# Optimization experiments

Measured on AMD Instinct MI355X. Metric: run time of the kernel, lower is better.

The kernel has to match this reference:

```python
import jax, jax.numpy as jnp
import numpy as np

B, CIN, H, W = 16, 256, 32, 32
COUT = 256
DK = 128       # key depth (total over heads)
DV = 128       # attentional channels (total over heads)
NH = 8
DKH = DK // NH # 16
DVH = DV // NH # 16
CCONV = COUT - DV  # channels of the plain conv branch


def setup_inputs() -> dict:
    key = jax.random.key(0)
    ks = jax.random.split(key, 7)
    x = jax.random.normal(ks[0], (B, CIN, H, W), dtype=jnp.float32)
    # 3x3 conv branch (padding=1), OIHW
    conv_w = jax.random.normal(ks[1], (CCONV, CIN, 3, 3), dtype=jnp.float32) * 0.02
    conv_b = jnp.zeros((CCONV,), dtype=jnp.float32)
    # 1x1 qkv conv, stored as [out, in]
    qkv_w = jax.random.normal(ks[2], (2 * DK + DV, CIN), dtype=jnp.float32) * 0.02
    qkv_b = jnp.zeros((2 * DK + DV,), dtype=jnp.float32)
    # 1x1 output projection for attention branch
    attn_w = jax.random.normal(ks[3], (DV, DV), dtype=jnp.float32) * 0.02
    attn_b = jnp.zeros((DV,), dtype=jnp.float32)
    return {"x": x, "conv_w": conv_w, "conv_b": conv_b,
            "qkv_w": qkv_w, "qkv_b": qkv_b,
            "attn_w": attn_w, "attn_b": attn_b}


def reference(x, conv_w, conv_b, qkv_w, qkv_b, attn_w, attn_b):
    b, _, h, w = x.shape
    hw = h * w
    # plain conv branch: 3x3, padding 1
    conv_out = jax.lax.conv_general_dilated(
        x, conv_w, window_strides=(1, 1), padding=((1, 1), (1, 1)),
        dimension_numbers=("NCHW", "OIHW", "NCHW")) + conv_b[None, :, None, None]
    # 1x1 qkv conv
    qkv = jnp.einsum("bchw,oc->bohw", x, qkv_w) + qkv_b[None, :, None, None]
    q = qkv[:, :DK].reshape(b, NH, DKH, hw) * (DKH ** -0.5)
    k = qkv[:, DK:2 * DK].reshape(b, NH, DKH, hw)
    v = qkv[:, 2 * DK:].reshape(b, NH, DVH, hw)
    # logits[b,n,p,q] = sum_c q[b,n,c,p] * k[b,n,c,q]
    logits = jnp.einsum("bncp,bncq->bnpq", q, k)
    weights = jax.nn.softmax(logits, axis=-1)
    # attn[b,n,c,p] = sum_q v[b,n,c,q] * weights[b,n,p,q]
    attn = jnp.einsum("bncq,bnpq->bncp", v, weights).reshape(b, DV, h, w)
    attn = jnp.einsum("bchw,oc->bohw", attn, attn_w) + attn_b[None, :, None, None]
    return jnp.concatenate((conv_out, attn), axis=1)
```

## Files before the change

kernel.cpp:

```cpp
#include <hip/hip_runtime.h>
#include <cstddef>

#define B_ 16
#define CIN_ 256
#define H_ 32
#define W_ 32
#define HW_ 1024
#define COUT_ 256
#define DK_ 128
#define DV_ 128
#define NH_ 8
#define DKH_ 16
#define DVH_ 16
#define CCONV_ 128
#define QKVO_ 384

typedef __attribute__((ext_vector_type(4))) _Float16 half4v;
typedef __attribute__((ext_vector_type(8))) _Float16 half8v;
typedef __attribute__((ext_vector_type(4))) float float4v;


__global__ __launch_bounds__(256) void xt_kernel(
    const float* __restrict__ x, _Float16* __restrict__ xF)
{
    const int pt = blockIdx.x;
    const int ct = blockIdx.y;
    const int b  = blockIdx.z;
    __shared__ float T[32][33];
    const int t = threadIdx.x;
    const int c = t & 31, r = t >> 5;
#pragma unroll
    for (int i = 0; i < 4; ++i) {
        const int ci = ct * 32 + r + i * 8;
        T[r + i * 8][c] = x[(size_t)(b * CIN_ + ci) * HW_ + pt * 32 + c];
    }
    __syncthreads();
    const int cq = (t & 7) * 4;
    const int pi = t >> 3;
    half4v h;
#pragma unroll
    for (int j = 0; j < 4; ++j) h[j] = (_Float16)T[cq + j][pi];
    const int p = pt * 32 + pi;
    *(half4v*)(xF + ((size_t)(b * 8 + ct) * HW_ + p) * 32 + cq) = h;
}

__global__ __launch_bounds__(256) void wprep_kernel(
    const float* __restrict__ conv_w, const float* __restrict__ qkv_w,
    const float* __restrict__ attn_w, _Float16* __restrict__ wC,
    _Float16* __restrict__ wF, _Float16* __restrict__ wP)
{
    const int bid = blockIdx.x;
    const int t = threadIdx.x;
    if (bid < 128) {
        const int id = bid * 256 + t;
        const int co = id >> 8, ci = id & 255;
        const float* src = conv_w + (size_t)id * 9;
#pragma unroll
        for (int j = 0; j < 9; ++j)
            wC[(((size_t)(ci >> 5) * 9 + j) * 8 + (co >> 4)) * 512 + (co & 15) * 32 + (ci & 31)]
                = (_Float16)src[j];
    } else if (bid < 224) {
        const int g = (bid - 128) * 256 + t;
        const int o = g >> 6, k0 = (g & 63) * 4;
        const float4 v = *(const float4*)(qkv_w + (size_t)o * CIN_ + k0);
        half4v h; h[0] = (_Float16)v.x; h[1] = (_Float16)v.y;
        h[2] = (_Float16)v.z; h[3] = (_Float16)v.w;
        *(half4v*)(wF + ((size_t)(k0 >> 5) * QKVO_ + o) * 32 + (k0 & 31)) = h;
    } else {
        const int g = (bid - 224) * 256 + t;
        const int o = g >> 5, k0 = (g & 31) * 4;
        const float4 v = *(const float4*)(attn_w + (size_t)o * DV_ + k0);
        half4v h; h[0] = (_Float16)v.x; h[1] = (_Float16)v.y;
        h[2] = (_Float16)v.z; h[3] = (_Float16)v.w;
        *(half4v*)(wP + ((size_t)(k0 >> 5) * DV_ + o) * 32 + (k0 & 31)) = h;
    }
}

__global__ __launch_bounds__(256) void qkv_kernel(
    const _Float16* __restrict__ xF, const _Float16* __restrict__ wF,
    const float* __restrict__ qkv_b, _Float16* __restrict__ Qt,
    _Float16* __restrict__ Kt, _Float16* __restrict__ vF)
{
    const int pt = blockIdx.x;
    const int ot = blockIdx.y;
    const int b  = blockIdx.z;
    const int lane = threadIdx.x & 63, w = threadIdx.x >> 6;
    const int l16 = lane & 15, hi = lane >> 4;
    const int p0 = pt * 64;
    const int og = ot * 4 + w;
    const int o0 = og * 16;

    float4v acc[4];
#pragma unroll
    for (int pg = 0; pg < 4; ++pg) acc[pg] = (float4v){0.f, 0.f, 0.f, 0.f};

    for (int kc = 0; kc < 8; ++kc) {
        const half8v a = *(const half8v*)(wF + ((size_t)kc * QKVO_ + o0 + l16) * 32 + hi * 8);
#pragma unroll
        for (int pg = 0; pg < 4; ++pg) {
            const half8v bf = *(const half8v*)(xF + ((size_t)(b * 8 + kc) * HW_ + p0 + pg * 16 + l16) * 32 + hi * 8);
            acc[pg] = __builtin_amdgcn_mfma_f32_16x16x32_f16(a, bf, acc[pg], 0, 0, 0);
        }
    }

    float bias[4];
#pragma unroll
    for (int r = 0; r < 4; ++r) bias[r] = qkv_b[o0 + hi * 4 + r];

    if (og < 16) {
        const float scale = (og < 8) ? 0.25f : 1.0f;
        const int n = og & 7;
        _Float16* dst = (og < 8 ? Qt : Kt) + (size_t)(b * NH_ + n) * (HW_ * 16) + hi * 4;
#pragma unroll
        for (int pg = 0; pg < 4; ++pg) {
            const int p = p0 + pg * 16 + l16;
            half4v h;
#pragma unroll
            for (int r = 0; r < 4; ++r) h[r] = (_Float16)((acc[pg][r] + bias[r]) * scale);
            *(half4v*)(dst + (size_t)p * 16) = h;
        }
    } else {
        const int n = og - 16;
        _Float16* Vb = vF + (size_t)(b * NH_ + n) * (64 * 16 * 16);
#pragma unroll
        for (int pg = 0; pg < 4; ++pg) {
            const int qg = pt * 4 + pg;
#pragma unroll
            for (int r = 0; r < 4; ++r)
                Vb[(size_t)(qg * 16 + hi * 4 + r) * 16 + l16] = (_Float16)(acc[pg][r] + bias[r]);
        }
    }
}

__global__ __launch_bounds__(256) void attn_kernel(
    const _Float16* __restrict__ Qt, const _Float16* __restrict__ Kt,
    const _Float16* __restrict__ vF, _Float16* __restrict__ aF)
{
    const int bx = blockIdx.x;
    const int pc = bx & 3;
    const int n  = (bx >> 2) & 7;
    const int b  = bx >> 5;
    const int lane = threadIdx.x & 63, wave = threadIdx.x >> 6;
    const int l16 = lane & 15, lg = lane >> 4;

    const int bn = b * NH_ + n;
    const _Float16* Qh = Qt + (size_t)bn * (HW_ * 16);
    const _Float16* Kh = Kt + (size_t)bn * (HW_ * 16);
    const _Float16* Vh = vF + (size_t)bn * (64 * 16 * 16);

    const int pbase = pc * 256 + wave * 64;

    half4v qf[4];
#pragma unroll
    for (int t = 0; t < 4; ++t)
        qf[t] = *(const half4v*)(Qh + (size_t)(pbase + t * 16 + l16) * 16 + lg * 4);

    float4v o[4];
    float rs[4];
#pragma unroll
    for (int t = 0; t < 4; ++t) { o[t] = (float4v){0.f, 0.f, 0.f, 0.f}; rs[t] = 0.f; }

    const float4v zero = (float4v){0.f, 0.f, 0.f, 0.f};

    for (int q0 = 0; q0 < HW_; q0 += 16) {
        const half4v kf = *(const half4v*)(Kh + (size_t)(q0 + l16) * 16 + lg * 4);
        const half4v vf = *(const half4v*)(Vh + (size_t)((q0 >> 4) * 16 + l16) * 16 + lg * 4);
#pragma unroll
        for (int t = 0; t < 4; ++t) {
            float4v s = __builtin_amdgcn_mfma_f32_16x16x16f16(kf, qf[t], zero, 0, 0, 0);
            const float e0 = __expf(s[0]);
            const float e1 = __expf(s[1]);
            const float e2 = __expf(s[2]);
            const float e3 = __expf(s[3]);
            rs[t] += (e0 + e1) + (e2 + e3);
            half4v pf;
            pf[0] = (_Float16)e0; pf[1] = (_Float16)e1;
            pf[2] = (_Float16)e2; pf[3] = (_Float16)e3;
            o[t] = __builtin_amdgcn_mfma_f32_16x16x16f16(vf, pf, o[t], 0, 0, 0);
        }
    }
#pragma unroll
    for (int t = 0; t < 4; ++t) {
        float r = rs[t];
        r += __shfl_xor(r, 16);
        r += __shfl_xor(r, 32);
        const float inv = 1.0f / r;
        half4v h;
#pragma unroll
        for (int rr = 0; rr < 4; ++rr) h[rr] = (_Float16)(o[t][rr] * inv);
        *(half4v*)(aF + (((size_t)(b * 64 + (pbase >> 4) + t) * 4 + (n >> 1)) * 16 + l16) * 32
                      + (n & 1) * 16 + lg * 4) = h;
    }
}

__global__ __launch_bounds__(256) void proj_kernel(
    const _Float16* __restrict__ aF, const _Float16* __restrict__ wP,
    const float* __restrict__ attn_b, float* __restrict__ out)
{
    const int pt = blockIdx.x;
    const int ot = blockIdx.y;
    const int b  = blockIdx.z;
    const int lane = threadIdx.x & 63, w = threadIdx.x >> 6;
    const int l16 = lane & 15, hi = lane >> 4;
    const int p0 = pt * 64;
    const int o0 = ot * 64 + w * 16;

    float4v acc[4];
#pragma unroll
    for (int pg = 0; pg < 4; ++pg) acc[pg] = (float4v){0.f, 0.f, 0.f, 0.f};

    for (int kc = 0; kc < 4; ++kc) {
        const half8v a = *(const half8v*)(wP + ((size_t)kc * DV_ + o0 + l16) * 32 + hi * 8);
#pragma unroll
        for (int pg = 0; pg < 4; ++pg) {
            const half8v bf = *(const half8v*)(aF + (((size_t)(b * 64 + pt * 4 + pg) * 4 + kc) * 16 + l16) * 32 + hi * 8);
            acc[pg] = __builtin_amdgcn_mfma_f32_16x16x32_f16(a, bf, acc[pg], 0, 0, 0);
        }
    }
#pragma unroll
    for (int pg = 0; pg < 4; ++pg) {
        const int p = p0 + pg * 16 + l16;
#pragma unroll
        for (int r = 0; r < 4; ++r) {
            const int o = o0 + hi * 4 + r;
            out[((size_t)(b * COUT_ + CCONV_ + o)) * HW_ + p] = acc[pg][r] + attn_b[o];
        }
    }
}

__global__ __launch_bounds__(256) void conv_kernel(
    const _Float16* __restrict__ xF, const _Float16* __restrict__ wC,
    const float* __restrict__ conv_b, float* __restrict__ out)
{
    const int rp = blockIdx.x;
    const int ch = blockIdx.y;
    const int b  = blockIdx.z;
    const int t = threadIdx.x;
    const int lane = t & 63, w = t >> 6;
    const int wc = w & 1, wp = w >> 1;
    const int l16 = lane & 15, hi = lane >> 4;
    const int r = rp * 2 + wp;
    const int coc0 = ch * 4 + wc * 2;

    const bool lane0bad  = (l16 == 0);
    const bool lane15bad = (l16 == 15);
    const half8v z = {0, 0, 0, 0, 0, 0, 0, 0};

    float4v acc[2][2];
#pragma unroll
    for (int i = 0; i < 2; ++i)
#pragma unroll
        for (int j = 0; j < 2; ++j) acc[i][j] = (float4v){0.f, 0.f, 0.f, 0.f};

    for (int kc = 0; kc < 8; ++kc) {
        const _Float16* xk = xF + ((size_t)(b * 8 + kc) * HW_ + r * 32) * 32 + l16 * 32 + hi * 8;
        const _Float16* ab = wC + ((size_t)(kc * 9) * 8 + coc0) * 512 + l16 * 32 + hi * 8;
#pragma unroll
        for (int kh = 0; kh < 3; ++kh) {
            const int rr = r + kh - 1;
            if ((unsigned)rr >= 32u) continue;
#pragma unroll
            for (int kw = 0; kw < 3; ++kw) {
                const _Float16* a = ab + (size_t)((kh * 3 + kw) * 8) * 512;
                const half8v a0 = *(const half8v*)(a);
                const half8v a1 = *(const half8v*)(a + 512);
                const int sh = ((kh - 1) * 32 + (kw - 1)) * 32;
                half8v b0 = *(const half8v*)(xk + sh);
                half8v b1 = *(const half8v*)(xk + sh + 16 * 32);
                if (kw == 0) b0 = lane0bad  ? z : b0;
                if (kw == 2) b1 = lane15bad ? z : b1;
                acc[0][0] = __builtin_amdgcn_mfma_f32_16x16x32_f16(a0, b0, acc[0][0], 0, 0, 0);
                acc[0][1] = __builtin_amdgcn_mfma_f32_16x16x32_f16(a0, b1, acc[0][1], 0, 0, 0);
                acc[1][0] = __builtin_amdgcn_mfma_f32_16x16x32_f16(a1, b0, acc[1][0], 0, 0, 0);
                acc[1][1] = __builtin_amdgcn_mfma_f32_16x16x32_f16(a1, b1, acc[1][1], 0, 0, 0);
            }
        }
    }
#pragma unroll
    for (int cog = 0; cog < 2; ++cog)
#pragma unroll
        for (int rr = 0; rr < 4; ++rr) {
            const int co = (coc0 + cog) * 16 + hi * 4 + rr;
            const float bias = conv_b[co];
            float* dst = out + (size_t)(b * COUT_ + co) * HW_ + r * 32;
            dst[l16]      = acc[cog][0][rr] + bias;
            dst[16 + l16] = acc[cog][1][rr] + bias;
        }
}

extern "C" void kernel_launch(void* const* d_in, const int* in_sizes, int n_in,
                              void* d_out, int out_size, void* d_ws, size_t ws_size,
                              hipStream_t stream)
{
    (void)in_sizes; (void)n_in; (void)out_size; (void)ws_size;
    const float* x      = (const float*)d_in[0];
    const float* conv_w = (const float*)d_in[1];
    const float* conv_b = (const float*)d_in[2];
    const float* qkv_w  = (const float*)d_in[3];
    const float* qkv_b  = (const float*)d_in[4];
    const float* attn_w = (const float*)d_in[5];
    const float* attn_b = (const float*)d_in[6];
    float* out = (float*)d_out;

    char* ws = (char*)d_ws;
    _Float16* xF = (_Float16*)(ws + 4096);
    _Float16* wC = (_Float16*)(ws + 8392704);
    _Float16* wF = (_Float16*)(ws + 8982528);
    _Float16* wP = (_Float16*)(ws + 9179136);
    _Float16* Qt = (_Float16*)(ws + 9211904);
    _Float16* Kt = (_Float16*)(ws + 13406208);
    _Float16* vF = (_Float16*)(ws + 17600512);
    _Float16* aF = (_Float16*)(ws + 21794816);

    xt_kernel<<<dim3(32, 8, B_), dim3(256), 0, stream>>>(x, xF);
    wprep_kernel<<<dim3(240), dim3(256), 0, stream>>>(conv_w, qkv_w, attn_w, wC, wF, wP);
    qkv_kernel<<<dim3(16, 6, B_), dim3(256), 0, stream>>>(xF, wF, qkv_b, Qt, Kt, vF);
    attn_kernel<<<dim3(512), dim3(256), 0, stream>>>(Qt, Kt, vF, aF);
    proj_kernel<<<dim3(16, 2, B_), dim3(256), 0, stream>>>(aF, wP, attn_b, out);
    conv_kernel<<<dim3(16, 2, B_), dim3(256), 0, stream>>>(xF, wC, conv_b, out);
}
```

Measured before the change: 177.3 us.

## Split attention keys across waves, use exp2 softmax, shrink conv tiles for more blocks

The attention kernel now splits the key dimension into two halves handled by paired waves, which doubles the grid to 1024 blocks. The partial outputs and row sums are combined through shared memory before normalization. Q is prescaled by log2(e)/4 so the native exp2 instruction replaces __expf. The conv kernel gives each wave a single 16-channel group on one row and doubles its grid, trading less weight and activation reuse per wave for more parallelism.

New measurement: 186.0 us. 4.9% more time.

```diff
diff --git a/kernel.cpp b/kernel.cpp
--- a/kernel.cpp
+++ b/kernel.cpp
@@ -19,6 +19,7 @@
 typedef __attribute__((ext_vector_type(8))) _Float16 half8v;
 typedef __attribute__((ext_vector_type(4))) float float4v;
 
+#define QSCALE 0.36067376022224085f
 
 __global__ __launch_bounds__(256) void xt_kernel(
     const float* __restrict__ x, _Float16* __restrict__ xF)
@@ -108,7 +109,7 @@
     for (int r = 0; r < 4; ++r) bias[r] = qkv_b[o0 + hi * 4 + r];
 
     if (og < 16) {
-        const float scale = (og < 8) ? 0.25f : 1.0f;
+        const float scale = (og < 8) ? QSCALE : 1.0f;
         const int n = og & 7;
         _Float16* dst = (og < 8 ? Qt : Kt) + (size_t)(b * NH_ + n) * (HW_ * 16) + hi * 4;
 #pragma unroll
@@ -137,10 +138,11 @@
     const _Float16* __restrict__ vF, _Float16* __restrict__ aF)
 {
     const int bx = blockIdx.x;
-    const int pc = bx & 3;
-    const int n  = (bx >> 2) & 7;
-    const int b  = bx >> 5;
+    const int pc = bx & 7;
+    const int n  = (bx >> 3) & 7;
+    const int b  = bx >> 6;
     const int lane = threadIdx.x & 63, wave = threadIdx.x >> 6;
+    const int pg = wave >> 1, qh = wave & 1;
     const int l16 = lane & 15, lg = lane >> 4;
 
     const int bn = b * NH_ + n;
@@ -148,7 +150,7 @@
     const _Float16* Kh = Kt + (size_t)bn * (HW_ * 16);
     const _Float16* Vh = vF + (size_t)bn * (64 * 16 * 16);
 
-    const int pbase = pc * 256 + wave * 64;
+    const int pbase = pc * 128 + pg * 64;
 
     half4v qf[4];
 #pragma unroll
@@ -162,16 +164,17 @@
 
     const float4v zero = (float4v){0.f, 0.f, 0.f, 0.f};
 
-    for (int q0 = 0; q0 < HW_; q0 += 16) {
+    const int q0beg = qh * 512;
+    for (int q0 = q0beg; q0 < q0beg + 512; q0 += 16) {
         const half4v kf = *(const half4v*)(Kh + (size_t)(q0 + l16) * 16 + lg * 4);
         const half4v vf = *(const half4v*)(Vh + (size_t)((q0 >> 4) * 16 + l16) * 16 + lg * 4);
 #pragma unroll
         for (int t = 0; t < 4; ++t) {
             float4v s = __builtin_amdgcn_mfma_f32_16x16x16f16(kf, qf[t], zero, 0, 0, 0);
-            const float e0 = __expf(s[0]);
-            const float e1 = __expf(s[1]);
-            const float e2 = __expf(s[2]);
-            const float e3 = __expf(s[3]);
+            const float e0 = __builtin_amdgcn_exp2f(s[0]);
+            const float e1 = __builtin_amdgcn_exp2f(s[1]);
+            const float e2 = __builtin_amdgcn_exp2f(s[2]);
+            const float e3 = __builtin_amdgcn_exp2f(s[3]);
             rs[t] += (e0 + e1) + (e2 + e3);
             half4v pf;
             pf[0] = (_Float16)e0; pf[1] = (_Float16)e1;
@@ -179,17 +182,37 @@
             o[t] = __builtin_amdgcn_mfma_f32_16x16x16f16(vf, pf, o[t], 0, 0, 0);
         }
     }
-#pragma unroll
-    for (int t = 0; t < 4; ++t) {
-        float r = rs[t];
-        r += __shfl_xor(r, 16);
-        r += __shfl_xor(r, 32);
-        const float inv = 1.0f / r;
-        half4v h;
-#pragma unroll
-        for (int rr = 0; rr < 4; ++rr) h[rr] = (_Float16)(o[t][rr] * inv);
-        *(half4v*)(aF + (((size_t)(b * 64 + (pbase >> 4) + t) * 4 + (n >> 1)) * 16 + l16) * 32
-                      + (n & 1) * 16 + lg * 4) = h;
+
+    __shared__ float Ored[2][64][16];
+    __shared__ float Rred[2][64][4];
+    if (qh == 1) {
+#pragma unroll
+        for (int t = 0; t < 4; ++t) {
+#pragma unroll
+            for (int rr = 0; rr < 4; ++rr) Ored[pg][lane][t * 4 + rr] = o[t][rr];
+            Rred[pg][lane][t] = rs[t];
+        }
+    }
+    __syncthreads();
+    if (qh == 0) {
+#pragma unroll
+        for (int t = 0; t < 4; ++t) {
+#pragma unroll
+            for (int rr = 0; rr < 4; ++rr) o[t][rr] += Ored[pg][lane][t * 4 + rr];
+            rs[t] += Rred[pg][lane][t];
+        }
+#pragma unroll
+        for (int t = 0; t < 4; ++t) {
+            float r = rs[t];
+            r += __shfl_xor(r, 16);
+            r += __shfl_xor(r, 32);
+            const float inv = 1.0f / r;
+            half4v h;
+#pragma unroll
+            for (int rr = 0; rr < 4; ++rr) h[rr] = (_Float16)(o[t][rr] * inv);
+            *(half4v*)(aF + (((size_t)(b * 64 + (pbase >> 4) + t) * 4 + (n >> 1)) * 16 + l16) * 32
+                          + (n & 1) * 16 + lg * 4) = h;
+        }
     }
 }
 
@@ -232,60 +255,50 @@
     const _Float16* __restrict__ xF, const _Float16* __restrict__ wC,
     const float* __restrict__ conv_b, float* __restrict__ out)
 {
-    const int rp = blockIdx.x;
+    const int r  = blockIdx.x;
     const int ch = blockIdx.y;
     const int b  = blockIdx.z;
     const int t = threadIdx.x;
     const int lane = t & 63, w = t >> 6;
-    const int wc = w & 1, wp = w >> 1;
     const int l16 = lane & 15, hi = lane >> 4;
-    const int r = rp * 2 + wp;
-    const int coc0 = ch * 4 + wc * 2;
+    const int c16 = ch * 4 + w;
 
     const bool lane0bad  = (l16 == 0);
     const bool lane15bad = (l16 == 15);
     const half8v z = {0, 0, 0, 0, 0, 0, 0, 0};
 
-    float4v acc[2][2];
-#pragma unroll
-    for (int i = 0; i < 2; ++i)
-#pragma unroll
-        for (int j = 0; j < 2; ++j) acc[i][j] = (float4v){0.f, 0.f, 0.f, 0.f};
+    float4v acc[2];
+    acc[0] = (float4v){0.f, 0.f, 0.f, 0.f};
+    acc[1] = (float4v){0.f, 0.f, 0.f, 0.f};
 
     for (int kc = 0; kc < 8; ++kc) {
         const _Float16* xk = xF + ((size_t)(b * 8 + kc) * HW_ + r * 32) * 32 + l16 * 32 + hi * 8;
-        const _Float16* ab = wC + ((size_t)(kc * 9) * 8 + coc0) * 512 + l16 * 32 + hi * 8;
+        const _Float16* ab = wC + ((size_t)(kc * 9) * 8 + c16) * 512 + l16 * 32 + hi * 8;
 #pragma unroll
         for (int kh = 0; kh < 3; ++kh) {
             const int rr = r + kh - 1;
             if ((unsigned)rr >= 32u) continue;
 #pragma unroll
             for (int kw = 0; kw < 3; ++kw) {
-                const _Float16* a = ab + (size_t)((kh * 3 + kw) * 8) * 512;
-                const half8v a0 = *(const half8v*)(a);
-                const half8v a1 = *(const half8v*)(a + 512);
+                const half8v a = *(const half8v*)(ab + (size_t)((kh * 3 + kw) * 8) * 512);
                 const int sh = ((kh - 1) * 32 + (kw - 1)) * 32;
                 half8v b0 = *(const half8v*)(xk + sh);
                 half8v b1 = *(const half8v*)(xk + sh + 16 * 32);
                 if (kw == 0) b0 = lane0bad  ? z : b0;
                 if (kw == 2) b1 = lane15bad ? z : b1;
-                acc[0][0] = __builtin_amdgcn_mfma_f32_16x16x32_f16(a0, b0, acc[0][0], 0, 0, 0);
-                acc[0][1] = __builtin_amdgcn_mfma_f32_16x16x32_f16(a0, b1, acc[0][1], 0, 0, 0);
-                acc[1][0] = __builtin_amdgcn_mfma_f32_16x16x32_f16(a1, b0, acc[1][0], 0, 0, 0);
-                acc[1][1] = __builtin_amdgcn_mfma_f32_16x16x32_f16(a1, b1, acc[1][1], 0, 0, 0);
+                acc[0] = __builtin_amdgcn_mfma_f32_16x16x32_f16(a, b0, acc[0], 0, 0, 0);
+                acc[1] = __builtin_amdgcn_mfma_f32_16x16x32_f16(a, b1, acc[1], 0, 0, 0);
             }
         }
     }
 #pragma unroll
-    for (int cog = 0; cog < 2; ++cog)
-#pragma unroll
-        for (int rr = 0; rr < 4; ++rr) {
-            const int co = (coc0 + cog) * 16 + hi * 4 + rr;
-            const float bias = conv_b[co];
-            float* dst = out + (size_t)(b * COUT_ + co) * HW_ + r * 32;
-            dst[l16]      = acc[cog][0][rr] + bias;
-            dst[16 + l16] = acc[cog][1][rr] + bias;
-        }
+    for (int rr = 0; rr < 4; ++rr) {
+        const int co = c16 * 16 + hi * 4 + rr;
+        const float bias = conv_b[co];
+        float* dst = out + (size_t)(b * COUT_ + co) * HW_ + r * 32;
+        dst[l16]      = acc[0][rr] + bias;
+        dst[16 + l16] = acc[1][rr] + bias;
+    }
 }
 
 extern "C" void kernel_launch(void* const* d_in, const int* in_sizes, int n_in,
@@ -315,7 +328,7 @@
     xt_kernel<<<dim3(32, 8, B_), dim3(256), 0, stream>>>(x, xF);
     wprep_kernel<<<dim3(240), dim3(256), 0, stream>>>(conv_w, qkv_w, attn_w, wC, wF, wP);
     qkv_kernel<<<dim3(16, 6, B_), dim3(256), 0, stream>>>(xF, wF, qkv_b, Qt, Kt, vF);
-    attn_kernel<<<dim3(512), dim3(256), 0, stream>>>(Qt, Kt, vF, aF);
+    attn_kernel<<<dim3(1024), dim3(256), 0, stream>>>(Qt, Kt, vF, aF);
     proj_kernel<<<dim3(16, 2, B_), dim3(256), 0, stream>>>(aF, wP, attn_b, out);
-    conv_kernel<<<dim3(16, 2, B_), dim3(256), 0, stream>>>(xF, wC, conv_b, out);
-}
+    conv_kernel<<<dim3(32, 2, B_), dim3(256), 0, stream>>>(xF, wC, conv_b, out);
+}
```
